# Optimization experiments

Hardware: AMD Instinct MI355X
Metric: run time of the kernel (lower is better)

Reference implementation:

```python
import jax, jax.numpy as jnp
import numpy as np

N, D, H, DATT, C, NCLS = 20000, 1024, 512, 256, 10, 4

def setup_inputs() -> dict:
    key = jax.random.key(0)
    ks = jax.random.split(key, 20)
    s = lambda fan_in: 1.0 / np.sqrt(fan_in)
    u = lambda k, shape, fan_in: jax.random.uniform(k, shape, jnp.float32, -s(fan_in), s(fan_in))
    inp = {
        'x': jax.random.normal(ks[0], (N, D), jnp.float32),
        'cluster_id': jax.random.randint(ks[1], (N,), 0, C),
        # per-cluster expert MLP (phi_i): Linear(D,H)+ReLU, Linear(H,H)+ReLU (dropout=identity in eval)
        'W1': u(ks[2], (C, D, H), D), 'b1': u(ks[3], (C, H), D),
        'W2': u(ks[4], (C, H, H), H), 'b2': u(ks[5], (C, H), H),
        # attention_net: Linear(H,H)+ReLU then gated attention (L=H, D=DATT, n_classes=1)
        'fc_W': u(ks[6], (H, H), H), 'fc_b': u(ks[7], (H,), H),
        'Wa': u(ks[8], (H, DATT), H), 'ba': u(ks[9], (DATT,), H),
        'Wb': u(ks[10], (H, DATT), H), 'bb': u(ks[11], (DATT,), H),
        'Wc': u(ks[12], (DATT, 1), DATT), 'bc': u(ks[13], (1,), DATT),
        # rho: Linear(H, DATT)+ReLU
        'rho_W': u(ks[14], (H, DATT), H), 'rho_b': u(ks[15], (DATT,), H),
        # classifier
        'cls_W': u(ks[16], (DATT, NCLS), DATT), 'cls_b': u(ks[17], (NCLS,), DATT),
    }
    return inp

def reference(x, cluster_id, W1, b1, W2, b2, fc_W, fc_b, Wa, ba, Wb, bb, Wc, bc, rho_W, rho_b, cls_W, cls_b):
    # --- per-cluster expert MLPs, vectorized over clusters (no python loop over data) ---
    # h1: [C, N, H] = ReLU(x @ W1_c + b1_c) for every cluster c
    h1 = jax.nn.relu(jnp.einsum('nd,cdh->cnh', x, W1) + b1[:, None, :])
    h2 = jax.nn.relu(jnp.einsum('cnh,chk->cnk', h1, W2) + b2[:, None, :])
    # masked mean-pool per cluster (AdaptiveAvgPool1d(1) over the cluster's tokens)
    mask = (cluster_id[None, :] == jnp.arange(C)[:, None]).astype(h2.dtype)  # [C, N]
    counts = jnp.maximum(mask.sum(axis=1), 1.0)                               # empty cluster -> zeros
    h_cluster = jnp.einsum('cn,cnh->ch', mask, h2) / counts[:, None]          # [C, H]
    # --- attention net: fc + gated attention ---
    h = jax.nn.relu(h_cluster @ fc_W + fc_b)                                  # [C, H]
    a = jnp.tanh(h @ Wa + ba)
    b = jax.nn.sigmoid(h @ Wb + bb)
    A = ((a * b) @ Wc + bc).T                                                 # [1, C]
    A = jax.nn.softmax(A, axis=1)
    h_path = A @ h                                                            # [1, H]
    hr = jax.nn.relu(h_path @ rho_W + rho_b)[0]                               # [DATT] (squeeze)
    logits = (hr @ cls_W + cls_b)[None, :]                                    # [1, NCLS]
    Y_prob = jax.nn.softmax(logits, axis=1)
    Y_hat = jnp.argmax(logits, axis=1, keepdims=True)
    return (logits, Y_prob, Y_hat)
```

## Files before the change

### kernel.cpp

```cpp
#include <hip/hip_runtime.h>
#include <hip/hip_bf16.h>
#include <stdint.h>

#define NT 20000
#define DIM 1024
#define HID 512
#define DATT_N 256
#define NCLUS 10
#define NCLS_N 4
#define NBS 79
#define NRT 157

typedef __bf16 bf16;
typedef __attribute__((ext_vector_type(8))) __bf16 bf16x8;
typedef __attribute__((ext_vector_type(4))) float f32x4;

__device__ __forceinline__ void gload_lds16(const void* g, void* l) {
  __builtin_amdgcn_global_load_lds(
      (const __attribute__((address_space(1))) unsigned int*)g,
      (__attribute__((address_space(3))) unsigned int*)l, 16, 0, 0);
}


#define TW1B (32 * 4 * NCLUS)
#define TW2B (16 * 4 * NCLUS)

__device__ __forceinline__ void tr_body(const float* __restrict__ s, bf16* __restrict__ d,
                                        int R, int Cc, int i0, int j0, float (*t)[128]) {
  int tid = threadIdx.x;
  int cr = tid >> 5;
  int cc4 = (tid & 31) << 2;
#pragma unroll
  for (int yy = 0; yy < 32; yy += 8)
    *(f32x4*)&t[yy + cr][cc4] = *(const f32x4*)&s[(size_t)(i0 + yy + cr) * Cc + j0 + cc4];
  __syncthreads();
  int col = tid >> 1, h = (tid & 1) << 4;
  bf16 tmp[16];
#pragma unroll
  for (int k = 0; k < 16; ++k) tmp[k] = (bf16)t[h + k][col];
  *(bf16x8*)&d[(size_t)(j0 + col) * R + i0 + h] = *(bf16x8*)&tmp[0];
  *(bf16x8*)&d[(size_t)(j0 + col) * R + i0 + h + 8] = *(bf16x8*)&tmp[8];
}

__global__ __launch_bounds__(256) void setup_kernel(
    const int* __restrict__ cid, int* __restrict__ blkcnt,
    const float* __restrict__ W1, bf16* __restrict__ w1t,
    const float* __restrict__ W2, bf16* __restrict__ w2t) {
  __shared__ float t[32][128];
  __shared__ int wcnt[4][16];
  int b = blockIdx.x;
  int tid = threadIdx.x;
  if (b < NBS) {
    int lane = tid & 63, w = tid >> 6;
    int n = b * 256 + tid;
    int mycid = (n < NT) ? cid[n] : -1;
#pragma unroll
    for (int c = 0; c < NCLUS; ++c) {
      unsigned long long m = __ballot(mycid == c);
      if (lane == c) wcnt[w][c] = __popcll(m);
    }
    __syncthreads();
    if (tid < NCLUS)
      blkcnt[b * NCLUS + tid] =
          wcnt[0][tid] + wcnt[1][tid] + wcnt[2][tid] + wcnt[3][tid];
  } else if (b < NBS + TW1B) {
    int bb = b - NBS;
    int z = bb >> 7, r = bb & 127, rt = r >> 2, ct = r & 3;
    tr_body(W1 + (size_t)z * DIM * HID, w1t + (size_t)z * DIM * HID,
            DIM, HID, rt * 32, ct * 128, t);
  } else {
    int bb = b - NBS - TW1B;
    int z = bb >> 6, r = bb & 63, rt = r >> 2, ct = r & 3;
    tr_body(W2 + (size_t)z * HID * HID, w2t + (size_t)z * HID * HID,
            HID, HID, rt * 32, ct * 128, t);
  }
}


#define ZPB 20

__global__ __launch_bounds__(256) void scatter_kernel(
    const int* __restrict__ cid, const int* __restrict__ blkcnt,
    int* __restrict__ cnt, int* __restrict__ offs, int* __restrict__ order,
    float* __restrict__ pool) {
  int tid = threadIdx.x;
  int bx = blockIdx.x;
  if (bx >= NBS) {
    int i = (bx - NBS) * 256 + tid;
    if (i < NCLUS * HID) pool[i] = 0.f;
    return;
  }
  __shared__ int sbase[16];
  __shared__ int scnt[16];
  __shared__ int soffs[16];
  __shared__ int wcnt[4][16];
  __shared__ int wbase[4][16];
  int lane = tid & 63, w = tid >> 6;
  if (tid < NCLUS) {
    int base = 0, run = 0;
    for (int b = 0; b < NBS; ++b) {
      int v = blkcnt[b * NCLUS + tid];
      if (b < bx) base += v;
      run += v;
    }
    sbase[tid] = base;
    scnt[tid] = run;
  }
  __syncthreads();
  if (tid == 0) {
    int a = 0;
    for (int i = 0; i < NCLUS; ++i) { soffs[i] = a; a += scnt[i]; }
    soffs[NCLUS] = a;
  }
  __syncthreads();
  if (bx == 0 && tid <= NCLUS) {
    if (tid < NCLUS) cnt[tid] = scnt[tid];
    offs[tid] = soffs[tid];
  }
  int n = bx * 256 + tid;
  int mycid = (n < NT) ? cid[n] : -1;
  unsigned long long lmask = (lane == 63) ? ~0ull >> 1 : (1ull << lane) - 1;
  int myrank = 0;
#pragma unroll
  for (int c = 0; c < NCLUS; ++c) {
    unsigned long long m = __ballot(mycid == c);
    if (mycid == c) myrank = __popcll(m & lmask);
    if (lane == c) wcnt[w][c] = __popcll(m);
  }
  __syncthreads();
  if (tid < NCLUS) {
    int pre = sbase[tid];
#pragma unroll
    for (int ww = 0; ww < 4; ++ww) { wbase[ww][tid] = pre; pre += wcnt[ww][tid]; }
  }
  __syncthreads();
  if (n < NT) order[soffs[mycid] + wbase[w][mycid] + myrank] = n;
}


__global__ __launch_bounds__(256) void gather_cast(
    const float* __restrict__ x, const int* __restrict__ order, bf16* __restrict__ xs) {
  int t = blockIdx.x * 256 + threadIdx.x;
  int row = t >> 6;
  if (row >= NT) return;
  int col = (t & 63) << 4;
  const f32x4* p = (const f32x4*)(x + (size_t)order[row] * DIM + col);
  f32x4 u0 = p[0], v0 = p[1], u1 = p[2], v1 = p[3];
  bf16x8 w0, w1;
  w0[0] = (bf16)u0[0]; w0[1] = (bf16)u0[1]; w0[2] = (bf16)u0[2]; w0[3] = (bf16)u0[3];
  w0[4] = (bf16)v0[0]; w0[5] = (bf16)v0[1]; w0[6] = (bf16)v0[2]; w0[7] = (bf16)v0[3];
  w1[0] = (bf16)u1[0]; w1[1] = (bf16)u1[1]; w1[2] = (bf16)u1[2]; w1[3] = (bf16)u1[3];
  w1[4] = (bf16)v1[0]; w1[5] = (bf16)v1[1]; w1[6] = (bf16)v1[2]; w1[7] = (bf16)v1[3];
  bf16* q = xs + (size_t)row * DIM + col;
  *(bf16x8*)q = w0;
  *(bf16x8*)(q + 8) = w1;
}

__device__ __forceinline__ bool decode_grp(int d, int& c, int& rt, int& j) {
  int x8 = d & 7, s = d >> 3;
  int g = (s >> 2) * 8 + x8;
  if (g >= NRT * NCLUS) return false;
  j = s & 3;
  c = g / NRT;
  rt = g - c * NRT;
  return true;
}


__global__ __launch_bounds__(256, 2) void gemm1_kernel(
    const bf16* __restrict__ xs, const bf16* __restrict__ w1t, const float* __restrict__ b1,
    const int* __restrict__ offs, const int* __restrict__ cnt, bf16* __restrict__ h1) {
  int c, rt, j;
  if (!decode_grp(blockIdx.x, c, rt, j)) return;
  int cntc = cnt[c];
  int row0 = rt * 128;
  if (row0 >= cntc) return;
  int seg = offs[c];
  int n0 = j * 128;

  __shared__ bf16 Als[128 * 64];
  __shared__ bf16 Bls[128 * 64];

  int tid = threadIdx.x;
  int lane = tid & 63, wid = tid >> 6;
  int wr = wid >> 1, wc = wid & 1;
  int rx = lane & 7, hi = lane >> 4;
  int kswz = ((lane & 7) ^ (lane >> 3)) << 3;

  const bf16* aptr[4]; int aoff[4];
  const bf16* bptr[4]; int boff[4];
#pragma unroll
  for (int i = 0; i < 4; ++i) {
    int chunk = i * 4 + wid;
    int r = chunk * 8 + (lane >> 3);
    int ar = seg + row0 + r; if (ar > NT - 1) ar = NT - 1;
    aptr[i] = xs + (size_t)ar * DIM + kswz;
    aoff[i] = chunk * 512;
    bptr[i] = w1t + (size_t)(c * HID + n0 + r) * DIM + kswz;
    boff[i] = chunk * 512;
  }

  f32x4 acc[4][4];
#pragma unroll
  for (int m = 0; m < 4; m++)
#pragma unroll
    for (int n = 0; n < 4; n++) acc[m][n] = {0.f, 0.f, 0.f, 0.f};

  for (int k0 = 0; k0 < DIM; k0 += 64) {
#pragma unroll
    for (int i = 0; i < 4; ++i) gload_lds16(aptr[i] + k0, &Als[aoff[i]]);
#pragma unroll
    for (int i = 0; i < 4; ++i) gload_lds16(bptr[i] + k0, &Bls[boff[i]]);
    __syncthreads();
#pragma unroll
    for (int ks = 0; ks < 2; ++ks) {
      int t16 = ks * 4 + hi;
      int ko = ((t16 ^ rx) << 3);
      bf16x8 a[4], b[4];
#pragma unroll
      for (int m = 0; m < 4; m++)
        a[m] = *(const bf16x8*)(&Als[(wr * 64 + m * 16 + (lane & 15)) * 64 + ko]);
#pragma unroll
      for (int n = 0; n < 4; n++)
        b[n] = *(const bf16x8*)(&Bls[(wc * 64 + n * 16 + (lane & 15)) * 64 + ko]);
#pragma unroll
      for (int m = 0; m < 4; m++)
#pragma unroll
        for (int n = 0; n < 4; n++)
          acc[m][n] = __builtin_amdgcn_mfma_f32_16x16x32_bf16(a[m], b[n], acc[m][n], 0, 0, 0);
    }
    __syncthreads();
  }

  int valid = cntc - row0; if (valid > 128) valid = 128;
#pragma unroll
  for (int n = 0; n < 4; n++) {
    int col = n0 + wc * 64 + n * 16 + (lane & 15);
    float bias = b1[c * HID + col];
#pragma unroll
    for (int m = 0; m < 4; m++) {
      int rbase = wr * 64 + m * 16 + ((lane >> 4) << 2);
#pragma unroll
      for (int e = 0; e < 4; e++) {
        int r = rbase + e;
        if (r < valid) {
          float v = acc[m][n][e] + bias;
          h1[(size_t)(seg + row0 + r) * HID + col] = (bf16)(v > 0.f ? v : 0.f);
        }
      }
    }
  }
}


__global__ __launch_bounds__(256, 2) void gemm2_kernel(
    const bf16* __restrict__ h1, const bf16* __restrict__ w2t, const float* __restrict__ b2,
    const int* __restrict__ offs, const int* __restrict__ cnt, float* __restrict__ pool) {
  int c, rt, j;
  if (!decode_grp(blockIdx.x, c, rt, j)) return;
  int cntc = cnt[c];
  int row0 = rt * 128;
  if (row0 >= cntc) return;
  int seg = offs[c];
  int n0 = j * 128;
  int valid = cntc - row0; if (valid > 128) valid = 128;

  __shared__ bf16 Als[128 * 64];
  __shared__ bf16 Bls[128 * 64];

  int tid = threadIdx.x;
  int lane = tid & 63, wid = tid >> 6;
  int wr = wid >> 1, wc = wid & 1;
  int rx = lane & 7, hi = lane >> 4;
  int kswz = ((lane & 7) ^ (lane >> 3)) << 3;

  const bf16* aptr[4]; int aoff[4];
  const bf16* bptr[4]; int boff[4];
#pragma unroll
  for (int i = 0; i < 4; ++i) {
    int chunk = i * 4 + wid;
    int r = chunk * 8 + (lane >> 3);
    int ar = seg + row0 + r; if (ar > NT - 1) ar = NT - 1;
    aptr[i] = h1 + (size_t)ar * HID + kswz;
    aoff[i] = chunk * 512;
    bptr[i] = w2t + (size_t)(c * HID + n0 + r) * HID + kswz;
    boff[i] = chunk * 512;
  }

  f32x4 acc[4][4];
#pragma unroll
  for (int m = 0; m < 4; m++)
#pragma unroll
    for (int n = 0; n < 4; n++) acc[m][n] = {0.f, 0.f, 0.f, 0.f};

  for (int k0 = 0; k0 < HID; k0 += 64) {
#pragma unroll
    for (int i = 0; i < 4; ++i) gload_lds16(aptr[i] + k0, &Als[aoff[i]]);
#pragma unroll
    for (int i = 0; i < 4; ++i) gload_lds16(bptr[i] + k0, &Bls[boff[i]]);
    __syncthreads();
#pragma unroll
    for (int ks = 0; ks < 2; ++ks) {
      int t16 = ks * 4 + hi;
      int ko = ((t16 ^ rx) << 3);
      bf16x8 a[4], b[4];
#pragma unroll
      for (int m = 0; m < 4; m++)
        a[m] = *(const bf16x8*)(&Als[(wr * 64 + m * 16 + (lane & 15)) * 64 + ko]);
#pragma unroll
      for (int n = 0; n < 4; n++)
        b[n] = *(const bf16x8*)(&Bls[(wc * 64 + n * 16 + (lane & 15)) * 64 + ko]);
#pragma unroll
      for (int m = 0; m < 4; m++)
#pragma unroll
        for (int n = 0; n < 4; n++)
          acc[m][n] = __builtin_amdgcn_mfma_f32_16x16x32_bf16(a[m], b[n], acc[m][n], 0, 0, 0);
    }
    __syncthreads();
  }

#pragma unroll
  for (int n = 0; n < 4; n++) {
    int col = n0 + wc * 64 + n * 16 + (lane & 15);
    float bias = b2[c * HID + col];
    float s = 0.f;
#pragma unroll
    for (int m = 0; m < 4; m++) {
      int rbase = wr * 64 + m * 16 + ((lane >> 4) << 2);
#pragma unroll
      for (int e = 0; e < 4; e++) {
        if (rbase + e < valid) {
          float v = acc[m][n][e] + bias;
          s += (v > 0.f ? v : 0.f);
        }
      }
    }
    s += __shfl_xor(s, 16);
    s += __shfl_xor(s, 32);
    if (lane < 16) atomicAdd(&pool[c * HID + n0 + wc * 64 + n * 16 + lane], s);
  }
}


__global__ __launch_bounds__(256) void tail_fc(
    const float* __restrict__ pool, const int* __restrict__ cnt,
    const float* __restrict__ fcW, const float* __restrict__ fcb,
    float* __restrict__ hbuf) {
  int c = blockIdx.x >> 3;
  int jt = blockIdx.x & 7;
  __shared__ float hc[HID];
  __shared__ float red[4][64];
  int tid = threadIdx.x;
  float inv = 1.f / fmaxf((float)cnt[c], 1.f);
  for (int k = tid; k < HID; k += 256) hc[k] = pool[c * HID + k] * inv;
  __syncthreads();
  int jl = tid & 63, kg = tid >> 6;
  int j = jt * 64 + jl;
  float s = 0.f;
#pragma unroll 4
  for (int k = kg * 128; k < kg * 128 + 128; ++k) s += hc[k] * fcW[(size_t)k * HID + j];
  red[kg][jl] = s;
  __syncthreads();
  if (kg == 0) {
    float v = red[0][jl] + red[1][jl] + red[2][jl] + red[3][jl] + fcb[j];
    hbuf[c * HID + j] = fmaxf(v, 0.f);
  }
}

__global__ __launch_bounds__(1024) void tail_att(
    const float* __restrict__ hbuf,
    const float* __restrict__ Wa, const float* __restrict__ ba,
    const float* __restrict__ Wb, const float* __restrict__ bb,
    const float* __restrict__ Wc, const float* __restrict__ bc,
    float* __restrict__ score) {
  int c = blockIdx.x;
  __shared__ float h[HID];
  __shared__ float ra[4][DATT_N];
  __shared__ float rb[4][DATT_N];
  __shared__ float sc[DATT_N];
  int tid = threadIdx.x;
  for (int k = tid; k < HID; k += 1024) h[k] = hbuf[c * HID + k];
  __syncthreads();
  int jl = tid & 255, kg = tid >> 8;
  float sa = 0.f, sb = 0.f;
#pragma unroll 4
  for (int k = kg * 128; k < kg * 128 + 128; ++k) {
    float hv = h[k];
    sa += hv * Wa[(size_t)k * DATT_N + jl];
    sb += hv * Wb[(size_t)k * DATT_N + jl];
  }
  ra[kg][jl] = sa;
  rb[kg][jl] = sb;
  __syncthreads();
  if (kg == 0) {
    float va = ra[0][jl] + ra[1][jl] + ra[2][jl] + ra[3][jl] + ba[jl];
    float vb = rb[0][jl] + rb[1][jl] + rb[2][jl] + rb[3][jl] + bb[jl];
    float av = tanhf(va);
    float bv = 1.f / (1.f + expf(-vb));
    sc[jl] = av * bv * Wc[jl];
  }
  __syncthreads();
  for (int s2 = 128; s2 > 0; s2 >>= 1) {
    if (tid < s2) sc[tid] += sc[tid + s2];
    __syncthreads();
  }
  if (tid == 0) score[c] = sc[0] + bc[0];
}

__global__ __launch_bounds__(1024) void tail_fin(
    const float* __restrict__ score, const float* __restrict__ hbuf,
    const float* __restrict__ rhoW, const float* __restrict__ rhob,
    const float* __restrict__ clsW, const float* __restrict__ clsb,
    float* __restrict__ out) {
  __shared__ float Asm[NCLUS];
  __shared__ float hp[HID];
  __shared__ float rr[4][DATT_N];
  __shared__ float hr[DATT_N];
  __shared__ float lg[NCLS_N];
  int tid = threadIdx.x;
  if (tid == 0) {
    float mx = -1e30f;
    for (int c = 0; c < NCLUS; c++) mx = fmaxf(mx, score[c]);
    float sum = 0.f, e[NCLUS];
    for (int c = 0; c < NCLUS; c++) { e[c] = expf(score[c] - mx); sum += e[c]; }
    for (int c = 0; c < NCLUS; c++) Asm[c] = e[c] / sum;
  }
  __syncthreads();
  if (tid < HID) {
    float s = 0.f;
#pragma unroll
    for (int c = 0; c < NCLUS; c++) s += Asm[c] * hbuf[c * HID + tid];
    hp[tid] = s;
  }
  __syncthreads();
  int jl = tid & 255, kg = tid >> 8;
  float s = 0.f;
#pragma unroll 4
  for (int k = kg * 128; k < kg * 128 + 128; ++k) s += hp[k] * rhoW[(size_t)k * DATT_N + jl];
  rr[kg][jl] = s;
  __syncthreads();
  if (kg == 0) hr[jl] = fmaxf(rr[0][jl] + rr[1][jl] + rr[2][jl] + rr[3][jl] + rhob[jl], 0.f);
  __syncthreads();
  if (tid < NCLS_N * 64) {
    int t = tid >> 6, l = tid & 63;
    float cs = 0.f;
    for (int j = l; j < DATT_N; j += 64) cs += hr[j] * clsW[j * NCLS_N + t];
#pragma unroll
    for (int w = 32; w > 0; w >>= 1) cs += __shfl_xor(cs, w);
    if (l == 0) lg[t] = cs + clsb[t];
  }
  __syncthreads();
  if (tid == 0) {
    float mx = lg[0];
    int am = 0;
    for (int t = 1; t < NCLS_N; t++) if (lg[t] > mx) { mx = lg[t]; am = t; }
    float sum = 0.f, e[NCLS_N];
    for (int t = 0; t < NCLS_N; t++) { e[t] = expf(lg[t] - mx); sum += e[t]; }
    for (int t = 0; t < NCLS_N; t++) {
      out[t] = lg[t];
      out[NCLS_N + t] = e[t] / sum;
    }
    out[2 * NCLS_N] = (float)am;
  }
}


extern "C" void kernel_launch(void* const* d_in, const int* in_sizes, int n_in,
                              void* d_out, int out_size, void* d_ws, size_t ws_size,
                              hipStream_t stream) {
  const float* x    = (const float*)d_in[0];
  const int*   cid  = (const int*)d_in[1];
  const float* W1   = (const float*)d_in[2];
  const float* b1   = (const float*)d_in[3];
  const float* W2   = (const float*)d_in[4];
  const float* b2   = (const float*)d_in[5];
  const float* fcW  = (const float*)d_in[6];
  const float* fcb  = (const float*)d_in[7];
  const float* Wa   = (const float*)d_in[8];
  const float* ba   = (const float*)d_in[9];
  const float* Wb   = (const float*)d_in[10];
  const float* bb   = (const float*)d_in[11];
  const float* Wc   = (const float*)d_in[12];
  const float* bc   = (const float*)d_in[13];
  const float* rhoW = (const float*)d_in[14];
  const float* rhob = (const float*)d_in[15];
  const float* clsW = (const float*)d_in[16];
  const float* clsb = (const float*)d_in[17];
  float* out = (float*)d_out;

  char* ws = (char*)d_ws;
  int*   cnt     = (int*)(ws + 0);
  int*   offs    = (int*)(ws + 64);
  float* score   = (float*)(ws + 128);
  int*   blkcnt  = (int*)(ws + 256);
  int*   order   = (int*)(ws + 256 + 4096);
  float* pool    = (float*)(ws + 256 + 4096 + 80000);
  float* hbuf    = (float*)(ws + 256 + 4096 + 80000 + NCLUS * HID * 4);
  size_t o = 256 + 4096 + 80000 + 2ull * NCLUS * HID * 4;
  o = (o + 255) & ~(size_t)255;
  bf16* w1t = (bf16*)(ws + o); o += (size_t)NCLUS * HID * DIM * 2;
  bf16* w2t = (bf16*)(ws + o); o += (size_t)NCLUS * HID * HID * 2;
  bf16* h1  = (bf16*)(ws + o); o += (size_t)NT * HID * 2;
  bf16* xs  = (bf16*)(ws + o); o += (size_t)NT * DIM * 2;

  setup_kernel<<<dim3(NBS + TW1B + TW2B), dim3(256), 0, stream>>>(
      cid, blkcnt, W1, w1t, W2, w2t);
  scatter_kernel<<<dim3(NBS + ZPB), dim3(256), 0, stream>>>(
      cid, blkcnt, cnt, offs, order, pool);
  gather_cast<<<dim3(NT * 64 / 256), dim3(256), 0, stream>>>(x, order, xs);

  int nblk = 8 * ((NRT * NCLUS + 7) / 8) * 4;
  gemm1_kernel<<<dim3(nblk), dim3(256), 0, stream>>>(xs, w1t, b1, offs, cnt, h1);
  gemm2_kernel<<<dim3(nblk), dim3(256), 0, stream>>>(h1, w2t, b2, offs, cnt, pool);

  tail_fc<<<dim3(NCLUS * 8), dim3(256), 0, stream>>>(pool, cnt, fcW, fcb, hbuf);
  tail_att<<<dim3(NCLUS), dim3(1024), 0, stream>>>(hbuf, Wa, ba, Wb, bb, Wc, bc, score);
  tail_fin<<<dim3(1), dim3(1024), 0, stream>>>(score, hbuf, rhoW, rhob, clsW, clsb, out);
}
```

Before: 129.5 us.

## Move row gather into gemm1 and split tail kernels across more blocks

The cast kernel now converts x to bf16 in its original row order, and gemm1 gathers A rows through a shared-memory copy of the order indices. This drops the dependence of the cast on the scatter result and makes the cast a plain streaming pass. The tail attention and rho stages are split over more, smaller blocks: attention scores are summed with atomics into a score buffer that scatter now zeroes, and the classifier becomes its own kernel. The cost is an extra launch and indirect A loads in gemm1 that may be less contiguous.

```diff
diff --git a/kernel.cpp b/kernel.cpp
--- a/kernel.cpp
+++ b/kernel.cpp
@@ -82,12 +82,13 @@
 __global__ __launch_bounds__(256) void scatter_kernel(
     const int* __restrict__ cid, const int* __restrict__ blkcnt,
     int* __restrict__ cnt, int* __restrict__ offs, int* __restrict__ order,
-    float* __restrict__ pool) {
+    float* __restrict__ pool, float* __restrict__ score) {
   int tid = threadIdx.x;
   int bx = blockIdx.x;
   if (bx >= NBS) {
     int i = (bx - NBS) * 256 + tid;
     if (i < NCLUS * HID) pool[i] = 0.f;
+    if (bx == NBS && tid < 16) score[tid] = 0.f;
     return;
   }
   __shared__ int sbase[16];
@@ -138,20 +139,19 @@
 }
 
 
-__global__ __launch_bounds__(256) void gather_cast(
-    const float* __restrict__ x, const int* __restrict__ order, bf16* __restrict__ xs) {
+__global__ __launch_bounds__(256) void cast_kernel(
+    const float* __restrict__ x, bf16* __restrict__ xs) {
   int t = blockIdx.x * 256 + threadIdx.x;
-  int row = t >> 6;
-  if (row >= NT) return;
-  int col = (t & 63) << 4;
-  const f32x4* p = (const f32x4*)(x + (size_t)order[row] * DIM + col);
+  size_t base = (size_t)t << 4;
+  if (base >= (size_t)NT * DIM) return;
+  const f32x4* p = (const f32x4*)(x + base);
   f32x4 u0 = p[0], v0 = p[1], u1 = p[2], v1 = p[3];
   bf16x8 w0, w1;
   w0[0] = (bf16)u0[0]; w0[1] = (bf16)u0[1]; w0[2] = (bf16)u0[2]; w0[3] = (bf16)u0[3];
   w0[4] = (bf16)v0[0]; w0[5] = (bf16)v0[1]; w0[6] = (bf16)v0[2]; w0[7] = (bf16)v0[3];
   w1[0] = (bf16)u1[0]; w1[1] = (bf16)u1[1]; w1[2] = (bf16)u1[2]; w1[3] = (bf16)u1[3];
   w1[4] = (bf16)v1[0]; w1[5] = (bf16)v1[1]; w1[6] = (bf16)v1[2]; w1[7] = (bf16)v1[3];
-  bf16* q = xs + (size_t)row * DIM + col;
+  bf16* q = xs + base;
   *(bf16x8*)q = w0;
   *(bf16x8*)(q + 8) = w1;
 }
@@ -168,7 +168,8 @@
 
 
 __global__ __launch_bounds__(256, 2) void gemm1_kernel(
-    const bf16* __restrict__ xs, const bf16* __restrict__ w1t, const float* __restrict__ b1,
+    const bf16* __restrict__ xs, const int* __restrict__ order,
+    const bf16* __restrict__ w1t, const float* __restrict__ b1,
     const int* __restrict__ offs, const int* __restrict__ cnt, bf16* __restrict__ h1) {
   int c, rt, j;
   if (!decode_grp(blockIdx.x, c, rt, j)) return;
@@ -180,9 +181,16 @@
 
   __shared__ bf16 Als[128 * 64];
   __shared__ bf16 Bls[128 * 64];
+  __shared__ int s_ord[128];
 
   int tid = threadIdx.x;
   int lane = tid & 63, wid = tid >> 6;
+  if (tid < 128) {
+    int ar = seg + row0 + tid; if (ar > NT - 1) ar = NT - 1;
+    s_ord[tid] = order[ar];
+  }
+  __syncthreads();
+
   int wr = wid >> 1, wc = wid & 1;
   int rx = lane & 7, hi = lane >> 4;
   int kswz = ((lane & 7) ^ (lane >> 3)) << 3;
@@ -193,8 +201,7 @@
   for (int i = 0; i < 4; ++i) {
     int chunk = i * 4 + wid;
     int r = chunk * 8 + (lane >> 3);
-    int ar = seg + row0 + r; if (ar > NT - 1) ar = NT - 1;
-    aptr[i] = xs + (size_t)ar * DIM + kswz;
+    aptr[i] = xs + (size_t)s_ord[r] * DIM + kswz;
     aoff[i] = chunk * 512;
     bptr[i] = w1t + (size_t)(c * HID + n0 + r) * DIM + kswz;
     boff[i] = chunk * 512;
@@ -367,56 +374,56 @@
   }
 }
 
-__global__ __launch_bounds__(1024) void tail_att(
+__global__ __launch_bounds__(256) void tail_att(
     const float* __restrict__ hbuf,
     const float* __restrict__ Wa, const float* __restrict__ ba,
     const float* __restrict__ Wb, const float* __restrict__ bb,
     const float* __restrict__ Wc, const float* __restrict__ bc,
     float* __restrict__ score) {
-  int c = blockIdx.x;
+  int c = blockIdx.x >> 2, js = blockIdx.x & 3;
   __shared__ float h[HID];
-  __shared__ float ra[4][DATT_N];
-  __shared__ float rb[4][DATT_N];
-  __shared__ float sc[DATT_N];
-  int tid = threadIdx.x;
-  for (int k = tid; k < HID; k += 1024) h[k] = hbuf[c * HID + k];
-  __syncthreads();
-  int jl = tid & 255, kg = tid >> 8;
+  __shared__ float ra[4][64];
+  __shared__ float rb[4][64];
+  __shared__ float sc[64];
+  int tid = threadIdx.x;
+  for (int k = tid; k < HID; k += 256) h[k] = hbuf[c * HID + k];
+  __syncthreads();
+  int jl = tid & 63, kg = tid >> 6;
+  int j = js * 64 + jl;
   float sa = 0.f, sb = 0.f;
 #pragma unroll 4
   for (int k = kg * 128; k < kg * 128 + 128; ++k) {
     float hv = h[k];
-    sa += hv * Wa[(size_t)k * DATT_N + jl];
-    sb += hv * Wb[(size_t)k * DATT_N + jl];
+    sa += hv * Wa[(size_t)k * DATT_N + j];
+    sb += hv * Wb[(size_t)k * DATT_N + j];
   }
   ra[kg][jl] = sa;
   rb[kg][jl] = sb;
   __syncthreads();
   if (kg == 0) {
-    float va = ra[0][jl] + ra[1][jl] + ra[2][jl] + ra[3][jl] + ba[jl];
-    float vb = rb[0][jl] + rb[1][jl] + rb[2][jl] + rb[3][jl] + bb[jl];
+    float va = ra[0][jl] + ra[1][jl] + ra[2][jl] + ra[3][jl] + ba[j];
+    float vb = rb[0][jl] + rb[1][jl] + rb[2][jl] + rb[3][jl] + bb[j];
     float av = tanhf(va);
     float bv = 1.f / (1.f + expf(-vb));
-    sc[jl] = av * bv * Wc[jl];
-  }
-  __syncthreads();
-  for (int s2 = 128; s2 > 0; s2 >>= 1) {
-    if (tid < s2) sc[tid] += sc[tid + s2];
-    __syncthreads();
-  }
-  if (tid == 0) score[c] = sc[0] + bc[0];
-}
-
-__global__ __launch_bounds__(1024) void tail_fin(
+    sc[jl] = av * bv * Wc[j];
+  }
+  __syncthreads();
+  if (tid < 64) {
+    float v = sc[tid];
+#pragma unroll
+    for (int w = 32; w > 0; w >>= 1) v += __shfl_xor(v, w);
+    if (tid == 0) atomicAdd(&score[c], v + (js == 0 ? bc[0] : 0.f));
+  }
+}
+
+__global__ __launch_bounds__(256) void tail_rho(
     const float* __restrict__ score, const float* __restrict__ hbuf,
     const float* __restrict__ rhoW, const float* __restrict__ rhob,
-    const float* __restrict__ clsW, const float* __restrict__ clsb,
-    float* __restrict__ out) {
+    float* __restrict__ hr) {
+  int blk = blockIdx.x;
   __shared__ float Asm[NCLUS];
   __shared__ float hp[HID];
-  __shared__ float rr[4][DATT_N];
-  __shared__ float hr[DATT_N];
-  __shared__ float lg[NCLS_N];
+  __shared__ float rr[8][32];
   int tid = threadIdx.x;
   if (tid == 0) {
     float mx = -1e30f;
@@ -426,21 +433,32 @@
     for (int c = 0; c < NCLUS; c++) Asm[c] = e[c] / sum;
   }
   __syncthreads();
-  if (tid < HID) {
+  for (int k = tid; k < HID; k += 256) {
     float s = 0.f;
 #pragma unroll
-    for (int c = 0; c < NCLUS; c++) s += Asm[c] * hbuf[c * HID + tid];
-    hp[tid] = s;
-  }
-  __syncthreads();
-  int jl = tid & 255, kg = tid >> 8;
+    for (int c = 0; c < NCLUS; c++) s += Asm[c] * hbuf[c * HID + k];
+    hp[k] = s;
+  }
+  __syncthreads();
+  int jl = tid & 31, kg = tid >> 5;
+  int j = blk * 32 + jl;
   float s = 0.f;
 #pragma unroll 4
-  for (int k = kg * 128; k < kg * 128 + 128; ++k) s += hp[k] * rhoW[(size_t)k * DATT_N + jl];
+  for (int k = kg * 64; k < kg * 64 + 64; ++k) s += hp[k] * rhoW[(size_t)k * DATT_N + j];
   rr[kg][jl] = s;
   __syncthreads();
-  if (kg == 0) hr[jl] = fmaxf(rr[0][jl] + rr[1][jl] + rr[2][jl] + rr[3][jl] + rhob[jl], 0.f);
-  __syncthreads();
+  if (kg == 0) {
+    float v = rr[0][jl] + rr[1][jl] + rr[2][jl] + rr[3][jl] +
+              rr[4][jl] + rr[5][jl] + rr[6][jl] + rr[7][jl] + rhob[j];
+    hr[j] = fmaxf(v, 0.f);
+  }
+}
+
+__global__ __launch_bounds__(256) void tail_cls(
+    const float* __restrict__ hr, const float* __restrict__ clsW,
+    const float* __restrict__ clsb, float* __restrict__ out) {
+  __shared__ float lg[NCLS_N];
+  int tid = threadIdx.x;
   if (tid < NCLS_N * 64) {
     int t = tid >> 6, l = tid & 63;
     float cs = 0.f;
@@ -492,11 +510,12 @@
   int*   cnt     = (int*)(ws + 0);
   int*   offs    = (int*)(ws + 64);
   float* score   = (float*)(ws + 128);
-  int*   blkcnt  = (int*)(ws + 256);
-  int*   order   = (int*)(ws + 256 + 4096);
-  float* pool    = (float*)(ws + 256 + 4096 + 80000);
-  float* hbuf    = (float*)(ws + 256 + 4096 + 80000 + NCLUS * HID * 4);
-  size_t o = 256 + 4096 + 80000 + 2ull * NCLUS * HID * 4;
+  float* hr      = (float*)(ws + 1024);
+  int*   blkcnt  = (int*)(ws + 4096);
+  int*   order   = (int*)(ws + 8192);
+  float* pool    = (float*)(ws + 8192 + 80000);
+  float* hbuf    = (float*)(ws + 8192 + 80000 + NCLUS * HID * 4);
+  size_t o = 8192 + 80000 + 2ull * NCLUS * HID * 4;
   o = (o + 255) & ~(size_t)255;
   bf16* w1t = (bf16*)(ws + o); o += (size_t)NCLUS * HID * DIM * 2;
   bf16* w2t = (bf16*)(ws + o); o += (size_t)NCLUS * HID * HID * 2;
@@ -506,14 +525,15 @@
   setup_kernel<<<dim3(NBS + TW1B + TW2B), dim3(256), 0, stream>>>(
       cid, blkcnt, W1, w1t, W2, w2t);
   scatter_kernel<<<dim3(NBS + ZPB), dim3(256), 0, stream>>>(
-      cid, blkcnt, cnt, offs, order, pool);
-  gather_cast<<<dim3(NT * 64 / 256), dim3(256), 0, stream>>>(x, order, xs);
+      cid, blkcnt, cnt, offs, order, pool, score);
+  cast_kernel<<<dim3(NT * 64 / 256), dim3(256), 0, stream>>>(x, xs);
 
   int nblk = 8 * ((NRT * NCLUS + 7) / 8) * 4;
-  gemm1_kernel<<<dim3(nblk), dim3(256), 0, stream>>>(xs, w1t, b1, offs, cnt, h1);
+  gemm1_kernel<<<dim3(nblk), dim3(256), 0, stream>>>(xs, order, w1t, b1, offs, cnt, h1);
   gemm2_kernel<<<dim3(nblk), dim3(256), 0, stream>>>(h1, w2t, b2, offs, cnt, pool);
 
   tail_fc<<<dim3(NCLUS * 8), dim3(256), 0, stream>>>(pool, cnt, fcW, fcb, hbuf);
-  tail_att<<<dim3(NCLUS), dim3(1024), 0, stream>>>(hbuf, Wa, ba, Wb, bb, Wc, bc, score);
-  tail_fin<<<dim3(1), dim3(1024), 0, stream>>>(score, hbuf, rhoW, rhob, clsW, clsb, out);
-}
+  tail_att<<<dim3(NCLUS * 4), dim3(256), 0, stream>>>(hbuf, Wa, ba, Wb, bb, Wc, bc, score);
+  tail_rho<<<dim3(8), dim3(256), 0, stream>>>(score, hbuf, rhoW, rhob, hr);
+  tail_cls<<<dim3(1), dim3(256), 0, stream>>>(hr, clsW, clsb, out);
+}
```

Result: faster. 126.0 us (-2.7%).
